# Kernel tuning notes

Measured on AMD Instinct MI355X. Metric: run time of the kernel, lower is better.

## Reference

```python
import jax, jax.numpy as jnp
import numpy as np

B, K, D, H, V = 4096, 64, 128, 2048, 10000
EPS = 1e-5


def _project_ball(x):
    # map arbitrary vectors strictly inside the unit Poincare ball
    n = jnp.linalg.norm(x, axis=-1, keepdims=True)
    return 0.9 * x / (1.0 + n)


def setup_inputs() -> dict:
    key = jax.random.key(0)
    ks = jax.random.split(key, 12)
    type_embeddings = _project_ball(jax.random.normal(ks[0], (B, D), jnp.float32))
    neighbor_indexes = jax.random.randint(ks[1], (B, K), 0, V, jnp.int32)
    one_hot_neighbor_types = jnp.round(jax.random.uniform(ks[2], (B, K), jnp.float32))
    frequencies = jax.random.randint(ks[3], (V,), 1, 100000).astype(jnp.float32)
    type_lut = _project_ball(jax.random.normal(ks[4], (V, D), jnp.float32))
    IN = D + K * (D + 4 + 1)  # 8640
    s = 0.02
    W1 = jax.random.normal(ks[5], (IN, H), jnp.float32) * s
    b1 = jnp.zeros((H,), jnp.float32)
    Wh1 = jax.random.normal(ks[6], (H, H), jnp.float32) * s
    bh1 = jnp.zeros((H,), jnp.float32)
    Wh2 = jax.random.normal(ks[7], (H, H), jnp.float32) * s
    bh2 = jnp.zeros((H,), jnp.float32)
    W2 = jax.random.normal(ks[8], (H, K), jnp.float32) * s
    b2 = jnp.zeros((K,), jnp.float32)
    return dict(type_embeddings=type_embeddings, neighbor_indexes=neighbor_indexes,
                one_hot_neighbor_types=one_hot_neighbor_types, frequencies=frequencies,
                type_lut=type_lut, W1=W1, b1=b1, Wh1=Wh1, bh1=bh1, Wh2=Wh2, bh2=bh2,
                W2=W2, b2=b2)


def _forward(type_embeddings, neighbor_indexes, one_hot_neighbor_types, frequencies,
             type_lut, W1, b1, Wh1, bh1, Wh2, bh2, W2, b2):
    # embedding gather: [B, K, D]
    v = type_lut[neighbor_indexes]
    u = type_embeddings[:, None, :]  # [B, 1, D] broadcasts against [B, K, D]

    # extra features, all [B, K]
    squ = jnp.sum(u * u, axis=-1)
    sqv = jnp.sum(v * v, axis=-1)
    diff = u - v
    sqdist = jnp.sum(diff * diff, axis=-1)
    x = 1.0 + 2.0 * sqdist / ((1.0 - squ) * (1.0 - sqv))
    x = jnp.maximum(x, 1.0 + EPS)
    poincare = jnp.log(x + jnp.sqrt(x * x - 1.0))  # arccosh(x)

    dot = jnp.sum(u * v, axis=-1)
    cos = dot / jnp.maximum(jnp.sqrt(squ) * jnp.sqrt(sqv), 1e-8)
    summ = u + v
    polarization = (jnp.sum(summ * summ, axis=-1) - sqdist) / 4.0

    popularity = jnp.log1p(frequencies[neighbor_indexes])  # vectorized gather + log1p

    extra = jnp.stack([poincare, cos, polarization, dot], axis=-1)  # [B, K, 4]
    neighbor_rep = jnp.concatenate([v, extra, popularity[..., None]], axis=-1)  # [B, K, D+5]
    neighbor_rep = neighbor_rep.reshape(type_embeddings.shape[0], -1)
    inp = jnp.concatenate([type_embeddings, neighbor_rep], axis=-1)  # [B, D+K*(D+5)]

    h = jax.nn.relu(inp @ W1 + b1)        # dropout is identity at eval
    h = jax.nn.relu(h @ Wh1 + bh1)
    h = jax.nn.relu(h @ Wh2 + bh2)
    logits = h @ W2 + b2                  # [B, K]
    distribution = jax.nn.sigmoid(logits)

    t = one_hot_neighbor_types
    # stable BCE-with-logits, mean reduction
    loss = jnp.mean(jnp.maximum(logits, 0.0) - logits * t + jnp.log1p(jnp.exp(-jnp.abs(logits))))
    return distribution, loss


def reference(type_embeddings, neighbor_indexes, one_hot_neighbor_types, frequencies,
              type_lut, W1, b1, Wh1, bh1, Wh2, bh2, W2, b2):
    return _forward(type_embeddings, neighbor_indexes, one_hot_neighbor_types, frequencies,
                    type_lut, W1, b1, Wh1, bh1, Wh2, bh2, W2, b2)
```

## Files before the change

kernel.cpp:

```cpp
#include <hip/hip_runtime.h>

typedef unsigned short u16;
typedef unsigned int   u32;
typedef __attribute__((ext_vector_type(8))) __bf16 bf16x8;
typedef __attribute__((ext_vector_type(4))) float  f32x4;
typedef __attribute__((ext_vector_type(4))) u32    u32x4;

#define AS1 __attribute__((address_space(1)))
#define AS3 __attribute__((address_space(3)))


__device__ __forceinline__ u16 f2bf(float f) {
  u32 u = __builtin_bit_cast(u32, f);
  u += 0x7fffu + ((u >> 16) & 1u);
  return (u16)(u >> 16);
}

__device__ __forceinline__ float wred(float v) {
#pragma unroll
  for (int off = 32; off > 0; off >>= 1) v += __shfl_xor(v, off, 64);
  return v;
}

__device__ __forceinline__ void stage16(const u16* g, u16* l) {
  __builtin_amdgcn_global_load_lds((const AS1 void*)g, (AS3 void*)l, 16, 0, 0);
}

__global__ __launch_bounds__(256) void feature_kernel(
    const float* __restrict__ te, const int* __restrict__ nidx,
    const float* __restrict__ freq, const float* __restrict__ lut,
    u16* __restrict__ inp)
{
  const int b = blockIdx.x;
  const int t = threadIdx.x;
  const int l = t & 63, w = t >> 6;
  __shared__ float u_sh[128];
  __shared__ float squ_sh;

  if (t < 128) u_sh[t] = te[(size_t)b * 128 + t];
  __syncthreads();
  if (w == 0) {
    float p = u_sh[l] * u_sh[l] + u_sh[l + 64] * u_sh[l + 64];
    p = wred(p);
    if (l == 0) squ_sh = p;
  }
  const size_t rb = (size_t)b * 8640;
  if (t < 64) {
    float2 u2 = *(const float2*)&u_sh[t * 2];
    u32 pk = (u32)f2bf(u2.x) | ((u32)f2bf(u2.y) << 16);
    *(u32*)&inp[rb + t * 2] = pk;
  }
  __syncthreads();

  const float squ = squ_sh;
  const float rsq = 1.0f - squ;
  const float2 u2 = *(const float2*)&u_sh[l * 2];

#pragma unroll
  for (int mk = 0; mk < 4; ++mk) {
    const int kbase = w * 16 + mk * 4;
    int idx[4]; float2 v2[4]; float sqv[4], dot[4];
#pragma unroll
    for (int j = 0; j < 4; j++) {
      idx[j] = nidx[b * 64 + kbase + j];
      v2[j] = *(const float2*)&lut[(size_t)idx[j] * 128 + l * 2];
    }
#pragma unroll
    for (int j = 0; j < 4; j++) {
      sqv[j] = v2[j].x * v2[j].x + v2[j].y * v2[j].y;
      dot[j] = u2.x * v2[j].x + u2.y * v2[j].y;
    }
#pragma unroll
    for (int off = 32; off > 0; off >>= 1) {
#pragma unroll
      for (int j = 0; j < 4; j++) {
        sqv[j] += __shfl_xor(sqv[j], off, 64);
        dot[j] += __shfl_xor(dot[j], off, 64);
      }
    }
#pragma unroll
    for (int j = 0; j < 4; j++) {
      u32 pk = (u32)f2bf(v2[j].x) | ((u32)f2bf(v2[j].y) << 16);
      *(u32*)&inp[rb + 128 + (size_t)(kbase + j) * 128 + l * 2] = pk;
    }
    float poin[4], cosv[4];
#pragma unroll
    for (int j = 0; j < 4; j++) {
      const float sqd = squ + sqv[j] - 2.0f * dot[j];
      float x = 1.0f + 2.0f * sqd / (rsq * (1.0f - sqv[j]));
      x = fmaxf(x, 1.0f + 1e-5f);
      poin[j] = logf(x + sqrtf(x * x - 1.0f));
      cosv[j] = dot[j] / fmaxf(sqrtf(squ * sqv[j]), 1e-8f);
    }
    if (l == 0) {
      u32x4 e0, e1;
#pragma unroll
      for (int j = 0; j < 2; j++) {
        e0[2 * j]     = (u32)f2bf(poin[j]) | ((u32)f2bf(cosv[j]) << 16);
        e0[2 * j + 1] = (u32)f2bf(dot[j])  | ((u32)f2bf(dot[j])  << 16);
        e1[2 * j]     = (u32)f2bf(poin[2 + j]) | ((u32)f2bf(cosv[2 + j]) << 16);
        e1[2 * j + 1] = (u32)f2bf(dot[2 + j])  | ((u32)f2bf(dot[2 + j])  << 16);
      }
      *(u32x4*)&inp[rb + 8320 + kbase * 4]     = e0;
      *(u32x4*)&inp[rb + 8320 + kbase * 4 + 8] = e1;
      u16 pp[4];
#pragma unroll
      for (int j = 0; j < 4; j++) pp[j] = f2bf(log1pf(freq[idx[j]]));
      *(u32*)&inp[rb + 8576 + kbase]     = (u32)pp[0] | ((u32)pp[1] << 16);
      *(u32*)&inp[rb + 8576 + kbase + 2] = (u32)pp[2] | ((u32)pp[3] << 16);
    }
  }
}

__device__ __forceinline__ int w1_orig_row(int p) {
  if (p < 128) return p;
  if (p < 8320) { int q = p - 128;  return 128 + (q >> 7) * 133 + (q & 127); }
  if (p < 8576) { int q = p - 8320; return 128 + (q >> 2) * 133 + 128 + (q & 3); }
  return 128 + (p - 8576) * 133 + 132;
}

__device__ __forceinline__ void w1_tile(const float* __restrict__ in,
                                        u16* __restrict__ out, int tile,
                                        u16 (*ls)[68], int t)
{
  const int p0 = (tile >> 5) << 6;
  const int h0 = (tile & 31) << 6;
  const int hl = t & 63, q = t >> 6;
#pragma unroll
  for (int i = 0; i < 16; i++) {
    int pl = i * 4 + q;
    int orig = w1_orig_row(p0 + pl);
    ls[hl][pl] = f2bf(in[(size_t)orig * 2048 + h0 + hl]);
  }
  __syncthreads();
  const int pp = t & 15, hq = t >> 4;
#pragma unroll
  for (int i = 0; i < 4; i++) {
    int hc = i * 16 + hq;
    uint2 vv = *(const uint2*)&ls[hc][pp * 4];
    *(uint2*)&out[(size_t)(h0 + hc) * 8640 + p0 + pp * 4] = vv;
  }
}

__device__ __forceinline__ void conv_tile(const float* __restrict__ in,
                                          u16* __restrict__ out, int R, int C,
                                          int tile, u16 (*ls)[68], int t)
{
  const int tiles_c = C >> 6;
  const int r0 = (tile / tiles_c) << 6;
  const int c0 = (tile % tiles_c) << 6;
  const int cl = t & 63, q = t >> 6;
#pragma unroll
  for (int i = 0; i < 16; i++) {
    int rl = i * 4 + q;
    ls[cl][rl] = f2bf(in[(size_t)(r0 + rl) * C + c0 + cl]);
  }
  __syncthreads();
  const int pp = t & 15, cq = t >> 4;
#pragma unroll
  for (int i = 0; i < 4; i++) {
    int cc = i * 16 + cq;
    uint2 vv = *(const uint2*)&ls[cc][pp * 4];
    *(uint2*)&out[(size_t)(c0 + cc) * R + r0 + pp * 4] = vv;
  }
}

__global__ __launch_bounds__(256) void transpose_all(
    const float* __restrict__ W1,  u16* __restrict__ w1t,
    const float* __restrict__ Wh1, u16* __restrict__ wh1t,
    const float* __restrict__ Wh2, u16* __restrict__ wh2t,
    const float* __restrict__ W2,  u16* __restrict__ w2t)
{
  __shared__ u16 ls[64][68];
  const int bid = blockIdx.x, t = threadIdx.x;
  if (bid < 4320)       w1_tile(W1, w1t, bid, ls, t);
  else if (bid < 5344)  conv_tile(Wh1, wh1t, 2048, 2048, bid - 4320, ls, t);
  else if (bid < 6368)  conv_tile(Wh2, wh2t, 2048, 2048, bid - 5344, ls, t);
  else                  conv_tile(W2,  w2t,  2048, 64,   bid - 6368, ls, t);
}

__global__ __launch_bounds__(256, 2) void gemm2b(
    const u16* __restrict__ A, const u16* __restrict__ BT,
    const float* __restrict__ bias, u16* __restrict__ out,
    int N, int Kd)
{
  extern __shared__ u16 lds[];
  const int t = threadIdx.x, l = t & 63, w = t >> 6;
  const int nb = N >> 7;
  const int cpx = gridDim.x >> 3;
  const int bid = (blockIdx.x & 7) * cpx + (blockIdx.x >> 3);
  const int bm = bid / nb, bn = bid % nb;
  const int m0 = bm << 7, n0 = bn << 7;
  const int vm = w >> 1, vn = w & 1;

  const size_t lda = (size_t)Kd;
  const int NT = Kd >> 6;

  const int sr = l >> 3;
  const int q  = (l & 7) ^ sr;
  const u16* sA = A  + (size_t)(m0 + w * 32 + sr) * lda + q * 8;
  const u16* sB = BT + (size_t)(n0 + w * 32 + sr) * lda + q * 8;
  const int dW = w * 2048;

  const int rl = l & 15;
  const int c0 = ((0 + (l >> 4)) ^ (rl & 7)) * 8;
  const int c1 = ((4 + (l >> 4)) ^ (rl & 7)) * 8;
  const int aBase = (vm * 64 + rl) * 64;
  const int bBase = 8192 + (vn * 64 + rl) * 64;

  f32x4 acc[4][4] = {};
  bf16x8 a0[4], a1[4], b0[4], b1[4];

  auto stageT = [&](int o, int tt) {
    const size_t kt = (size_t)tt * 64;
#pragma unroll
    for (int i = 0; i < 4; i++) {
      stage16(sA + (size_t)i * 8 * lda + kt, lds + o + dW + i * 512);
      stage16(sB + (size_t)i * 8 * lda + kt, lds + o + 8192 + dW + i * 512);
    }
  };
  auto mmq = [&](const bf16x8* a, const bf16x8* b) {
    __builtin_amdgcn_s_setprio(1);
#pragma unroll
    for (int mi = 0; mi < 4; mi++)
#pragma unroll
      for (int ni = 0; ni < 4; ni++)
        acc[mi][ni] = __builtin_amdgcn_mfma_f32_16x16x32_bf16(a[mi], b[ni], acc[mi][ni], 0, 0, 0);
    __builtin_amdgcn_s_setprio(0);
  };

  stageT(0, 0);

  for (int ti = 0; ti < NT; ++ti) {
    const int o  = (ti & 1) ? 16384 : 0;
    const int on = o ^ 16384;
    asm volatile("s_waitcnt vmcnt(0)" ::: "memory");
    __builtin_amdgcn_s_barrier();
    if (ti + 1 < NT) stageT(on, ti + 1);
#pragma unroll
    for (int x = 0; x < 4; x++) b0[x] = *(const bf16x8*)&lds[o + bBase + x * 1024 + c0];
#pragma unroll
    for (int x = 0; x < 4; x++) a0[x] = *(const bf16x8*)&lds[o + aBase + x * 1024 + c0];
#pragma unroll
    for (int x = 0; x < 4; x++) b1[x] = *(const bf16x8*)&lds[o + bBase + x * 1024 + c1];
#pragma unroll
    for (int x = 0; x < 4; x++) a1[x] = *(const bf16x8*)&lds[o + aBase + x * 1024 + c1];
    asm volatile("s_waitcnt lgkmcnt(8)" ::: "memory");
    __builtin_amdgcn_sched_barrier(0);
    mmq(a0, b0);
    asm volatile("s_waitcnt lgkmcnt(0)" ::: "memory");
    __builtin_amdgcn_sched_barrier(0);
    mmq(a1, b1);
  }

  const int rq = l >> 4, rl2 = l & 15;
#pragma unroll
  for (int mi = 0; mi < 4; mi++) {
#pragma unroll
    for (int ni = 0; ni < 4; ni++) {
      const int col = n0 + vn * 64 + ni * 16 + rl2;
      const float bv = bias[col];
#pragma unroll
      for (int j = 0; j < 4; j++) {
        const int row = m0 + vm * 64 + mi * 16 + rq * 4 + j;
        float vv = acc[mi][ni][j] + bv;
        out[(size_t)row * N + col] = f2bf(fmaxf(vv, 0.0f));
      }
    }
  }
}

__global__ __launch_bounds__(256, 2) void gemm4_part(
    const u16* __restrict__ A, const u16* __restrict__ BT,
    float* __restrict__ pbuf)
{
  __shared__ u16 lsA[2 * 128 * 32];
  __shared__ u16 lsB[2 * 64 * 32];
  const int t = threadIdx.x, l = t & 63, w = t >> 6;
  const int bmx = blockIdx.x & 31, sk = blockIdx.x >> 5;
  const int m0 = bmx << 7, k0 = sk << 9;
  float* pout = pbuf + (size_t)sk * 262144;
  const int wm = w >> 1, wn = w & 1;

  f32x4 acc[4][2] = {};
  const int srow = l >> 2, scol = (l & 3) * 8;

  const u16* pA0 = A  + (size_t)(m0 + w * 16 + srow)      * 2048 + scol + k0;
  const u16* pA1 = A  + (size_t)(m0 + 64 + w * 16 + srow) * 2048 + scol + k0;
  const u16* pB0 = BT + (size_t)(w * 16 + srow)           * 2048 + scol + k0;

  auto stage = [&](int buf, int kt) {
    u16* dA = lsA + buf * 4096;
    u16* dB = lsB + buf * 2048;
    stage16(pA0 + kt, dA + w * 512);
    stage16(pA1 + kt, dA + 2048 + w * 512);
    stage16(pB0 + kt, dB + w * 512);
  };

  stage(0, 0);
  __syncthreads();

  const int kk = (l >> 4) * 8;
  const int rl = l & 15;
  int cur = 0;
  for (int kt = 0; kt < 512; kt += 32) {
    if (kt + 32 < 512) stage(cur ^ 1, kt + 32);
    const u16* sA = lsA + cur * 4096;
    const u16* sB = lsB + cur * 2048;
    bf16x8 a[4], bb[2];
#pragma unroll
    for (int mi = 0; mi < 4; mi++)
      a[mi] = *(const bf16x8*)&sA[(wm * 64 + mi * 16 + rl) * 32 + kk];
#pragma unroll
    for (int ni = 0; ni < 2; ni++)
      bb[ni] = *(const bf16x8*)&sB[(wn * 32 + ni * 16 + rl) * 32 + kk];
#pragma unroll
    for (int mi = 0; mi < 4; mi++)
#pragma unroll
      for (int ni = 0; ni < 2; ni++)
        acc[mi][ni] = __builtin_amdgcn_mfma_f32_16x16x32_bf16(a[mi], bb[ni], acc[mi][ni], 0, 0, 0);
    __syncthreads();
    cur ^= 1;
  }

  const int rq = l >> 4, rl2 = l & 15;
#pragma unroll
  for (int mi = 0; mi < 4; mi++)
#pragma unroll
    for (int ni = 0; ni < 2; ni++) {
      const int col = wn * 32 + ni * 16 + rl2;
#pragma unroll
      for (int j = 0; j < 4; j++) {
        const int row = m0 + wm * 64 + mi * 16 + rq * 4 + j;
        pout[(size_t)row * 64 + col] = acc[mi][ni][j];
      }
    }
}

__global__ __launch_bounds__(256) void gemm4_combine(
    const float* __restrict__ pbuf, const float* __restrict__ bias,
    const float* __restrict__ oneh, float* __restrict__ dist,
    float* __restrict__ part2)
{
  __shared__ float red[256];
  const int t = threadIdx.x;
  const size_t base = (size_t)blockIdx.x * 1024 + t * 4;
  f32x4 s = *(const f32x4*)&pbuf[base];
  s += *(const f32x4*)&pbuf[base + 262144];
  s += *(const f32x4*)&pbuf[base + 524288];
  s += *(const f32x4*)&pbuf[base + 786432];
  const int col0 = (int)(base & 63);
  f32x4 th = *(const f32x4*)&oneh[base];
  float lsum = 0.0f;
  f32x4 dv;
#pragma unroll
  for (int j = 0; j < 4; j++) {
    const float x = s[j] + bias[col0 + j];
    dv[j] = 1.0f / (1.0f + expf(-x));
    lsum += fmaxf(x, 0.0f) - x * th[j] + log1pf(expf(-fabsf(x)));
  }
  *(f32x4*)&dist[base] = dv;
  red[t] = lsum;
  __syncthreads();
  for (int s2 = 128; s2 > 0; s2 >>= 1) {
    if (t < s2) red[t] += red[t + s2];
    __syncthreads();
  }
  if (t == 0) part2[blockIdx.x] = red[0];
}

__global__ void loss_final(const float* __restrict__ part2, float* __restrict__ outloss) {
  const int l = threadIdx.x;
  float v = 0.0f;
#pragma unroll
  for (int i = 0; i < 4; i++) v += part2[l + i * 64];
  v = wred(v);
  if (l == 0) outloss[0] = v * (1.0f / 262144.0f);
}

extern "C" void kernel_launch(void* const* d_in, const int* in_sizes, int n_in,
                              void* d_out, int out_size, void* d_ws, size_t ws_size,
                              hipStream_t stream)
{
  const float* te   = (const float*)d_in[0];
  const int*   nidx = (const int*)  d_in[1];
  const float* oneh = (const float*)d_in[2];
  const float* freq = (const float*)d_in[3];
  const float* lut  = (const float*)d_in[4];
  const float* W1   = (const float*)d_in[5];
  const float* b1   = (const float*)d_in[6];
  const float* Wh1  = (const float*)d_in[7];
  const float* bh1  = (const float*)d_in[8];
  const float* Wh2  = (const float*)d_in[9];
  const float* bh2  = (const float*)d_in[10];
  const float* W2   = (const float*)d_in[11];
  const float* b2   = (const float*)d_in[12];

  float* dist  = (float*)d_out;
  float* lossp = dist + 262144;

  size_t off = 0;
  char* base = (char*)d_ws;
  auto alloc = [&](size_t bytes) { char* p = base + off; off += (bytes + 255) & ~(size_t)255; return p; };
  u16* inp   = (u16*)alloc((size_t)4096 * 8640 * 2);
  u16* w1t   = (u16*)alloc((size_t)2048 * 8640 * 2);
  u16* wh1t  = (u16*)alloc((size_t)2048 * 2048 * 2);
  u16* wh2t  = (u16*)alloc((size_t)2048 * 2048 * 2);
  u16* w2t   = (u16*)alloc((size_t)64 * 2048 * 2);
  u16* h1    = (u16*)alloc((size_t)4096 * 2048 * 2);
  float* part2 = (float*)alloc(1024);
  u16* h2 = inp;
  u16* h3 = w1t;
  float* pbuf = (float*)wh1t;
  if (off > ws_size) return;

  (void)hipFuncSetAttribute((const void*)gemm2b,
                            hipFuncAttributeMaxDynamicSharedMemorySize, 65536);

  feature_kernel<<<4096, 256, 0, stream>>>(te, nidx, freq, lut, inp);
  transpose_all<<<6400, 256, 0, stream>>>(W1, w1t, Wh1, wh1t, Wh2, wh2t, W2, w2t);

  gemm2b<<<512, 256, 65536, stream>>>(inp, w1t, b1, h1, 2048, 8640);
  gemm2b<<<512, 256, 65536, stream>>>(h1, wh1t, bh1, h2, 2048, 2048);
  gemm2b<<<512, 256, 65536, stream>>>(h2, wh2t, bh2, h3, 2048, 2048);
  gemm4_part   <<<128, 256, 0, stream>>>(h3, w2t, pbuf);
  gemm4_combine<<<256, 256, 0, stream>>>(pbuf, b2, oneh, dist, part2);
  loss_final   <<<1, 64, 0, stream>>>(part2, lossp);
}
```

Baseline: 326.1 us.

## Triple-buffer GEMM with BK=32 and merge feature and transpose kernels

```diff
diff --git a/kernel.cpp b/kernel.cpp
--- a/kernel.cpp
+++ b/kernel.cpp
@@ -26,17 +26,79 @@
   __builtin_amdgcn_global_load_lds((const AS1 void*)g, (AS3 void*)l, 16, 0, 0);
 }
 
-__global__ __launch_bounds__(256) void feature_kernel(
+__device__ __forceinline__ int w1_orig_row(int p) {
+  if (p < 128) return p;
+  if (p < 8320) { int q = p - 128;  return 128 + (q >> 7) * 133 + (q & 127); }
+  if (p < 8576) { int q = p - 8320; return 128 + (q >> 2) * 133 + 128 + (q & 3); }
+  return 128 + (p - 8576) * 133 + 132;
+}
+
+__device__ __forceinline__ void w1_tile(const float* __restrict__ in,
+                                        u16* __restrict__ out, int tile,
+                                        u16 (*ls)[68], int t)
+{
+  const int p0 = (tile >> 5) << 6;
+  const int h0 = (tile & 31) << 6;
+  const int hl = t & 63, q = t >> 6;
+#pragma unroll
+  for (int i = 0; i < 16; i++) {
+    int pl = i * 4 + q;
+    int orig = w1_orig_row(p0 + pl);
+    ls[hl][pl] = f2bf(in[(size_t)orig * 2048 + h0 + hl]);
+  }
+  __syncthreads();
+  const int pp = t & 15, hq = t >> 4;
+#pragma unroll
+  for (int i = 0; i < 4; i++) {
+    int hc = i * 16 + hq;
+    uint2 vv = *(const uint2*)&ls[hc][pp * 4];
+    *(uint2*)&out[(size_t)(h0 + hc) * 8640 + p0 + pp * 4] = vv;
+  }
+}
+
+__device__ __forceinline__ void conv_tile(const float* __restrict__ in,
+                                          u16* __restrict__ out, int R, int C,
+                                          int tile, u16 (*ls)[68], int t)
+{
+  const int tiles_c = C >> 6;
+  const int r0 = (tile / tiles_c) << 6;
+  const int c0 = (tile % tiles_c) << 6;
+  const int cl = t & 63, q = t >> 6;
+#pragma unroll
+  for (int i = 0; i < 16; i++) {
+    int rl = i * 4 + q;
+    ls[cl][rl] = f2bf(in[(size_t)(r0 + rl) * C + c0 + cl]);
+  }
+  __syncthreads();
+  const int pp = t & 15, cq = t >> 4;
+#pragma unroll
+  for (int i = 0; i < 4; i++) {
+    int cc = i * 16 + cq;
+    uint2 vv = *(const uint2*)&ls[cc][pp * 4];
+    *(uint2*)&out[(size_t)(c0 + cc) * R + r0 + pp * 4] = vv;
+  }
+}
+
+__global__ __launch_bounds__(256) void prep_kernel(
+    const float* __restrict__ W1,  u16* __restrict__ w1t,
+    const float* __restrict__ Wh1, u16* __restrict__ wh1t,
+    const float* __restrict__ Wh2, u16* __restrict__ wh2t,
+    const float* __restrict__ W2,  u16* __restrict__ w2t,
     const float* __restrict__ te, const int* __restrict__ nidx,
     const float* __restrict__ freq, const float* __restrict__ lut,
     u16* __restrict__ inp)
 {
-  const int b = blockIdx.x;
-  const int t = threadIdx.x;
-  const int l = t & 63, w = t >> 6;
+  __shared__ u16 ls[64][68];
   __shared__ float u_sh[128];
   __shared__ float squ_sh;
-
+  const int bid = blockIdx.x, t = threadIdx.x;
+  if (bid < 4320)      { w1_tile(W1, w1t, bid, ls, t); return; }
+  if (bid < 5344)      { conv_tile(Wh1, wh1t, 2048, 2048, bid - 4320, ls, t); return; }
+  if (bid < 6368)      { conv_tile(Wh2, wh2t, 2048, 2048, bid - 5344, ls, t); return; }
+  if (bid < 6400)      { conv_tile(W2,  w2t,  2048, 64,   bid - 6368, ls, t); return; }
+
+  const int b = bid - 6400;
+  const int l = t & 63, w = t >> 6;
   if (t < 128) u_sh[t] = te[(size_t)b * 128 + t];
   __syncthreads();
   if (w == 0) {
@@ -112,73 +174,6 @@
   }
 }
 
-__device__ __forceinline__ int w1_orig_row(int p) {
-  if (p < 128) return p;
-  if (p < 8320) { int q = p - 128;  return 128 + (q >> 7) * 133 + (q & 127); }
-  if (p < 8576) { int q = p - 8320; return 128 + (q >> 2) * 133 + 128 + (q & 3); }
-  return 128 + (p - 8576) * 133 + 132;
-}
-
-__device__ __forceinline__ void w1_tile(const float* __restrict__ in,
-                                        u16* __restrict__ out, int tile,
-                                        u16 (*ls)[68], int t)
-{
-  const int p0 = (tile >> 5) << 6;
-  const int h0 = (tile & 31) << 6;
-  const int hl = t & 63, q = t >> 6;
-#pragma unroll
-  for (int i = 0; i < 16; i++) {
-    int pl = i * 4 + q;
-    int orig = w1_orig_row(p0 + pl);
-    ls[hl][pl] = f2bf(in[(size_t)orig * 2048 + h0 + hl]);
-  }
-  __syncthreads();
-  const int pp = t & 15, hq = t >> 4;
-#pragma unroll
-  for (int i = 0; i < 4; i++) {
-    int hc = i * 16 + hq;
-    uint2 vv = *(const uint2*)&ls[hc][pp * 4];
-    *(uint2*)&out[(size_t)(h0 + hc) * 8640 + p0 + pp * 4] = vv;
-  }
-}
-
-__device__ __forceinline__ void conv_tile(const float* __restrict__ in,
-                                          u16* __restrict__ out, int R, int C,
-                                          int tile, u16 (*ls)[68], int t)
-{
-  const int tiles_c = C >> 6;
-  const int r0 = (tile / tiles_c) << 6;
-  const int c0 = (tile % tiles_c) << 6;
-  const int cl = t & 63, q = t >> 6;
-#pragma unroll
-  for (int i = 0; i < 16; i++) {
-    int rl = i * 4 + q;
-    ls[cl][rl] = f2bf(in[(size_t)(r0 + rl) * C + c0 + cl]);
-  }
-  __syncthreads();
-  const int pp = t & 15, cq = t >> 4;
-#pragma unroll
-  for (int i = 0; i < 4; i++) {
-    int cc = i * 16 + cq;
-    uint2 vv = *(const uint2*)&ls[cc][pp * 4];
-    *(uint2*)&out[(size_t)(c0 + cc) * R + r0 + pp * 4] = vv;
-  }
-}
-
-__global__ __launch_bounds__(256) void transpose_all(
-    const float* __restrict__ W1,  u16* __restrict__ w1t,
-    const float* __restrict__ Wh1, u16* __restrict__ wh1t,
-    const float* __restrict__ Wh2, u16* __restrict__ wh2t,
-    const float* __restrict__ W2,  u16* __restrict__ w2t)
-{
-  __shared__ u16 ls[64][68];
-  const int bid = blockIdx.x, t = threadIdx.x;
-  if (bid < 4320)       w1_tile(W1, w1t, bid, ls, t);
-  else if (bid < 5344)  conv_tile(Wh1, wh1t, 2048, 2048, bid - 4320, ls, t);
-  else if (bid < 6368)  conv_tile(Wh2, wh2t, 2048, 2048, bid - 5344, ls, t);
-  else                  conv_tile(W2,  w2t,  2048, 64,   bid - 6368, ls, t);
-}
-
 __global__ __launch_bounds__(256, 2) void gemm2b(
     const u16* __restrict__ A, const u16* __restrict__ BT,
     const float* __restrict__ bias, u16* __restrict__ out,
@@ -194,32 +189,43 @@
   const int vm = w >> 1, vn = w & 1;
 
   const size_t lda = (size_t)Kd;
-  const int NT = Kd >> 6;
-
-  const int sr = l >> 3;
-  const int q  = (l & 7) ^ sr;
-  const u16* sA = A  + (size_t)(m0 + w * 32 + sr) * lda + q * 8;
-  const u16* sB = BT + (size_t)(n0 + w * 32 + sr) * lda + q * 8;
-  const int dW = w * 2048;
-
-  const int rl = l & 15;
-  const int c0 = ((0 + (l >> 4)) ^ (rl & 7)) * 8;
-  const int c1 = ((4 + (l >> 4)) ^ (rl & 7)) * 8;
-  const int aBase = (vm * 64 + rl) * 64;
-  const int bBase = 8192 + (vn * 64 + rl) * 64;
+  const int NT = Kd >> 5;
+
+  const int sr4 = l >> 2;
+  const int q4  = (l & 3) ^ (sr4 & 3);
+  const u16* sA = A  + (size_t)(m0 + w * 32 + sr4) * lda + q4 * 8;
+  const u16* sB = BT + (size_t)(n0 + w * 32 + sr4) * lda + q4 * 8;
+
+  const int rl  = l & 15;
+  const int swz = (((l >> 4)) ^ (rl & 3)) * 8;
+  const int aOff = (vm * 64 + rl) * 32 + swz;
+  const int bOff = 4096 + (vn * 64 + rl) * 32 + swz;
 
   f32x4 acc[4][4] = {};
-  bf16x8 a0[4], a1[4], b0[4], b1[4];
+  bf16x8 a[4], b[4];
 
   auto stageT = [&](int o, int tt) {
-    const size_t kt = (size_t)tt * 64;
-#pragma unroll
-    for (int i = 0; i < 4; i++) {
-      stage16(sA + (size_t)i * 8 * lda + kt, lds + o + dW + i * 512);
-      stage16(sB + (size_t)i * 8 * lda + kt, lds + o + 8192 + dW + i * 512);
-    }
+    const size_t kt = (size_t)tt * 32;
+    stage16(sA + kt,            lds + o + (w * 2) * 512);
+    stage16(sA + 16 * lda + kt, lds + o + (w * 2 + 1) * 512);
+    stage16(sB + kt,            lds + o + 4096 + (w * 2) * 512);
+    stage16(sB + 16 * lda + kt, lds + o + 4096 + (w * 2 + 1) * 512);
   };
-  auto mmq = [&](const bf16x8* a, const bf16x8* b) {
+
+  int o0 = 0, o1 = 8192, o2 = 16384;
+  stageT(o0, 0);
+  if (NT > 1) stageT(o1, 1);
+  asm volatile("s_waitcnt vmcnt(4)" ::: "memory");
+  __builtin_amdgcn_s_barrier();
+
+  for (int ti = 0; ti < NT; ++ti) {
+    if (ti + 2 < NT) stageT(o2, ti + 2);
+#pragma unroll
+    for (int x = 0; x < 4; x++) b[x] = *(const bf16x8*)&lds[o0 + bOff + x * 512];
+#pragma unroll
+    for (int x = 0; x < 4; x++) a[x] = *(const bf16x8*)&lds[o0 + aOff + x * 512];
+    asm volatile("s_waitcnt lgkmcnt(0)" ::: "memory");
+    __builtin_amdgcn_sched_barrier(0);
     __builtin_amdgcn_s_setprio(1);
 #pragma unroll
     for (int mi = 0; mi < 4; mi++)
@@ -227,30 +233,10 @@
       for (int ni = 0; ni < 4; ni++)
         acc[mi][ni] = __builtin_amdgcn_mfma_f32_16x16x32_bf16(a[mi], b[ni], acc[mi][ni], 0, 0, 0);
     __builtin_amdgcn_s_setprio(0);
-  };
-
-  stageT(0, 0);
-
-  for (int ti = 0; ti < NT; ++ti) {
-    const int o  = (ti & 1) ? 16384 : 0;
-    const int on = o ^ 16384;
-    asm volatile("s_waitcnt vmcnt(0)" ::: "memory");
+    if (ti + 2 < NT) asm volatile("s_waitcnt vmcnt(4)" ::: "memory");
+    else             asm volatile("s_waitcnt vmcnt(0)" ::: "memory");
     __builtin_amdgcn_s_barrier();
-    if (ti + 1 < NT) stageT(on, ti + 1);
-#pragma unroll
-    for (int x = 0; x < 4; x++) b0[x] = *(const bf16x8*)&lds[o + bBase + x * 1024 + c0];
-#pragma unroll
-    for (int x = 0; x < 4; x++) a0[x] = *(const bf16x8*)&lds[o + aBase + x * 1024 + c0];
-#pragma unroll
-    for (int x = 0; x < 4; x++) b1[x] = *(const bf16x8*)&lds[o + bBase + x * 1024 + c1];
-#pragma unroll
-    for (int x = 0; x < 4; x++) a1[x] = *(const bf16x8*)&lds[o + aBase + x * 1024 + c1];
-    asm volatile("s_waitcnt lgkmcnt(8)" ::: "memory");
-    __builtin_amdgcn_sched_barrier(0);
-    mmq(a0, b0);
-    asm volatile("s_waitcnt lgkmcnt(0)" ::: "memory");
-    __builtin_amdgcn_sched_barrier(0);
-    mmq(a1, b1);
+    const int tmp = o0; o0 = o1; o1 = o2; o2 = tmp;
   }
 
   const int rq = l >> 4, rl2 = l & 15;
@@ -415,14 +401,14 @@
   if (off > ws_size) return;
 
   (void)hipFuncSetAttribute((const void*)gemm2b,
-                            hipFuncAttributeMaxDynamicSharedMemorySize, 65536);
-
-  feature_kernel<<<4096, 256, 0, stream>>>(te, nidx, freq, lut, inp);
-  transpose_all<<<6400, 256, 0, stream>>>(W1, w1t, Wh1, wh1t, Wh2, wh2t, W2, w2t);
-
-  gemm2b<<<512, 256, 65536, stream>>>(inp, w1t, b1, h1, 2048, 8640);
-  gemm2b<<<512, 256, 65536, stream>>>(h1, wh1t, bh1, h2, 2048, 2048);
-  gemm2b<<<512, 256, 65536, stream>>>(h2, wh2t, bh2, h3, 2048, 2048);
+                            hipFuncAttributeMaxDynamicSharedMemorySize, 49152);
+
+  prep_kernel<<<10496, 256, 0, stream>>>(W1, w1t, Wh1, wh1t, Wh2, wh2t, W2, w2t,
+                                         te, nidx, freq, lut, inp);
+
+  gemm2b<<<512, 256, 49152, stream>>>(inp, w1t, b1, h1, 2048, 8640);
+  gemm2b<<<512, 256, 49152, stream>>>(h1, wh1t, bh1, h2, 2048, 2048);
+  gemm2b<<<512, 256, 49152, stream>>>(h2, wh2t, bh2, h3, 2048, 2048);
   gemm4_part   <<<128, 256, 0, stream>>>(h3, w2t, pbuf);
   gemm4_combine<<<256, 256, 0, stream>>>(pbuf, b2, oneh, dist, part2);
   loss_final   <<<1, 64, 0, stream>>>(part2, lossp);
```

Measured after the change: 374.7 us. 1.15x slower.
